# Optimization experiments

Measured on AMD Instinct MI355X. Metric: run time of the kernel, lower is better.

## Reference

```python
import jax, jax.numpy as jnp
import numpy as np

B, S, D_MODEL = 2, 2048, 2048
N_HEADS, N_KV_HEADS = 32, 8
HEAD_DIM = D_MODEL // N_HEADS  # 64


def setup_inputs() -> dict:
    key = jax.random.key(0)
    ks = jax.random.split(key, 7)
    # rope frequencies (as in standard RoPE; values just need to be the right shape)
    inv_freq = 1.0 / (10000.0 ** (jnp.arange(0, HEAD_DIM, 2, dtype=jnp.float32) / HEAD_DIM))
    t = jnp.arange(S, dtype=jnp.float32)
    freqs = t[:, None] * inv_freq[None, :]  # (S, head_dim//2)
    scale = 0.02
    return {
        "x": jax.random.normal(ks[0], (B, S, D_MODEL), jnp.float32),
        "cos": jnp.cos(freqs),
        "sin": jnp.sin(freqs),
        "Wq": jax.random.normal(ks[1], (N_HEADS * HEAD_DIM, D_MODEL), jnp.float32) * scale,
        "Wk": jax.random.normal(ks[2], (N_KV_HEADS * HEAD_DIM, D_MODEL), jnp.float32) * scale,
        "Wv": jax.random.normal(ks[3], (N_KV_HEADS * HEAD_DIM, D_MODEL), jnp.float32) * scale,
        "Wo": jax.random.normal(ks[4], (D_MODEL, D_MODEL), jnp.float32) * scale,
    }


def _apply_rope(x, cos, sin):
    # x: (B, H, S, D); cos/sin: (S, D//2)
    d = x.shape[-1]
    x1, x2 = x[..., : d // 2], x[..., d // 2:]
    c = cos[None, None]
    s = sin[None, None]
    return jnp.concatenate([x1 * c - x2 * s, x1 * s + x2 * c], axis=-1)


def reference(x, cos, sin, Wq, Wk, Wv, Wo):
    b, s, _ = x.shape
    hd = 2 * cos.shape[-1]
    h = Wq.shape[0] // hd
    kv = Wk.shape[0] // hd
    g = h // kv  # query heads per kv head

    q = (x @ Wq.T).reshape(b, s, h, hd).transpose(0, 2, 1, 3)    # (b,h,s,d)
    k = (x @ Wk.T).reshape(b, s, kv, hd).transpose(0, 2, 1, 3)   # (b,kv,s,d)
    v = (x @ Wv.T).reshape(b, s, kv, hd).transpose(0, 2, 1, 3)

    q = _apply_rope(q, cos, sin)
    k = _apply_rope(k, cos, sin)

    # GQA: group query heads instead of materializing repeated K/V
    qg = q.reshape(b, kv, g, s, hd)
    scale = 1.0 / jnp.sqrt(jnp.asarray(hd, x.dtype))
    scores = jnp.einsum('bkgsd,bktd->bkgst', qg, k) * scale      # (b,kv,g,s,s)
    causal = jnp.arange(s)[:, None] >= jnp.arange(s)[None, :]
    scores = jnp.where(causal[None, None, None], scores, jnp.asarray(-jnp.inf, scores.dtype))
    attn = jax.nn.softmax(scores, axis=-1)
    out = jnp.einsum('bkgst,bktd->bkgsd', attn, v)               # (b,kv,g,s,d)
    out = out.reshape(b, h, s, hd).transpose(0, 2, 1, 3).reshape(b, s, h * hd)
    return out @ Wo.T
```

## Files before the change

### kernel.cpp

```cpp
#include <hip/hip_runtime.h>
#include <hip/hip_bf16.h>

typedef __bf16 bf16;
typedef __attribute__((ext_vector_type(8))) __bf16 bf16x8;
typedef __attribute__((ext_vector_type(4))) __bf16 bf16x4;
typedef __attribute__((ext_vector_type(4))) float f32x4;

#define B_SZ 2
#define S_SZ 2048
#define D_SZ 2048
#define H_SZ 32
#define KV_SZ 8
#define HD_SZ 64
#define M_SZ (B_SZ * S_SZ)
#define NQKV 3072

#define GLDS(g, s) __builtin_amdgcn_global_load_lds( \
    (const __attribute__((address_space(1))) void*)(g), \
    (__attribute__((address_space(3))) void*)(s), 16, 0, 0)

__global__ void cvt_all(const float* __restrict__ x, const float* __restrict__ Wq,
                        const float* __restrict__ Wk, const float* __restrict__ Wv,
                        bf16* __restrict__ xb, bf16* __restrict__ Wf,
                        int nx, int n1, int n2) {
    int i = blockIdx.x * blockDim.x + threadIdx.x;
    const float* src; bf16* dst; int off;
    if (i < nx)                { src = x;  dst = xb; off = i; }
    else {
        int j = i - nx;
        if (j < n1)            { src = Wq; dst = Wf; off = j; }
        else if (j < n1 + n2)  { src = Wk; dst = Wf + (size_t)4 * n1; off = j - n1; }
        else if (j < n1+2*n2)  { src = Wv; dst = Wf + (size_t)4 * (n1 + n2); off = j - n1 - n2; }
        else return;
    }
    float4 v = ((const float4*)src)[off];
    bf16x4 o;
    o.x = (bf16)v.x; o.y = (bf16)v.y; o.z = (bf16)v.z; o.w = (bf16)v.w;
    ((bf16x4*)dst)[off] = o;
}

__global__ void cvt_f32_bf16(const float* __restrict__ in, bf16* __restrict__ out, int n4) {
    int i = blockIdx.x * blockDim.x + threadIdx.x;
    if (i >= n4) return;
    float4 v = ((const float4*)in)[i];
    bf16x4 o;
    o.x = (bf16)v.x; o.y = (bf16)v.y; o.z = (bf16)v.z; o.w = (bf16)v.w;
    ((bf16x4*)out)[i] = o;
}

#define BK 64

#define GEMM_CORE(A_, B_, Kdim)                                                  \
    const int g8 = lane >> 3;                                                    \
    const int chs = ((lane & 7) ^ g8) * 8;                                       \
    const bf16* Ag = A_ + (size_t)(rowBase + g8) * Kdim + chs;                   \
    const bf16* Bg = B_ + (size_t)(colBase + g8) * Kdim + chs;                   \
    f32x4 acc[4][4] = {};                                                        \
    for (int k0 = 0; k0 < Kdim; k0 += BK) {                                      \
        _Pragma("unroll")                                                        \
        for (int j = 0; j < 4; j++) {                                            \
            int is = wave * 4 + j;                                               \
            GLDS(Ag + (size_t)(is * 8) * Kdim + k0, As + is * 512);              \
            GLDS(Bg + (size_t)(is * 8) * Kdim + k0, Bs + is * 512);              \
        }                                                                        \
        __syncthreads();                                                         \
        _Pragma("unroll")                                                        \
        for (int ks = 0; ks < 2; ks++) {                                         \
            bf16x8 af[4], bfr[4];                                                \
            _Pragma("unroll")                                                    \
            for (int mi = 0; mi < 4; mi++)                                       \
                af[mi] = *(const bf16x8*)(As + (waveM * 64 + mi * 16 + c) * 64   \
                                          + (((ks << 2) + quad) ^ (c & 7)) * 8); \
            _Pragma("unroll")                                                    \
            for (int ni = 0; ni < 4; ni++)                                       \
                bfr[ni] = *(const bf16x8*)(Bs + (waveN * 64 + ni * 16 + c) * 64  \
                                          + (((ks << 2) + quad) ^ (c & 7)) * 8); \
            _Pragma("unroll")                                                    \
            for (int mi = 0; mi < 4; mi++)                                       \
                _Pragma("unroll")                                                \
                for (int ni = 0; ni < 4; ni++)                                   \
                    acc[mi][ni] = __builtin_amdgcn_mfma_f32_16x16x32_bf16(       \
                        af[mi], bfr[ni], acc[mi][ni], 0, 0, 0);                  \
        }                                                                        \
        __syncthreads();                                                         \
    }

__global__ __launch_bounds__(256)
void gemm_qkv(const bf16* __restrict__ A, const bf16* __restrict__ Bw,
              bf16* __restrict__ Qb, bf16* __restrict__ Kb, bf16* __restrict__ Vtb,
              const float* __restrict__ cosp, const float* __restrict__ sinp,
              float qscale)
{
    __shared__ __align__(16) bf16 As[128 * BK];
    __shared__ __align__(16) bf16 Bs[128 * BK];
    const int tid  = threadIdx.x;
    const int lane = tid & 63;
    const int wave = tid >> 6;
    const int waveM = wave >> 1, waveN = wave & 1;
    const int c = lane & 15, quad = lane >> 4;
    const int rowBase = blockIdx.y * 128;
    const int colBase = blockIdx.x * 128;

    GEMM_CORE(A, Bw, D_SZ)

    const int mBase = rowBase + waveM * 64;
    const int nBase = colBase + waveN * 64;

    if (nBase < 2560) {
        bf16* dst; int hh, Hn; float sc;
        if (nBase < 2048) { dst = Qb; hh = nBase >> 6;        Hn = H_SZ;  sc = qscale; }
        else              { dst = Kb; hh = (nBase >> 6) - 32; Hn = KV_SZ; sc = 1.0f;  }
#pragma unroll
        for (int mi = 0; mi < 4; mi++) {
#pragma unroll
            for (int r = 0; r < 4; r++) {
                int row = mBase + mi * 16 + quad * 4 + r;
                int b = row >> 11;
                int s = row & 2047;
                const float* cr = cosp + (size_t)s * 32;
                const float* sr = sinp + (size_t)s * 32;
                size_t base = ((size_t)(b * Hn + hh) * S_SZ + s) * 64;
#pragma unroll
                for (int ni = 0; ni < 2; ni++) {
                    int d = ni * 16 + c;
                    float x1 = acc[mi][ni][r];
                    float x2 = acc[mi][ni + 2][r];
                    float cv = cr[d], sv = sr[d];
                    dst[base + d]      = (bf16)((x1 * cv - x2 * sv) * sc);
                    dst[base + d + 32] = (bf16)((x1 * sv + x2 * cv) * sc);
                }
            }
        }
    } else {
        const int kvh = (nBase >> 6) - 40;
        const int b   = mBase >> 11;
        const int s0  = mBase & 2047;
#pragma unroll
        for (int ni = 0; ni < 4; ni++) {
            int d = ni * 16 + c;
            size_t base = ((size_t)(b * KV_SZ + kvh) * 64 + d) * (size_t)S_SZ;
#pragma unroll
            for (int mi = 0; mi < 4; mi++) {
                int s = s0 + mi * 16 + quad * 4;
#pragma unroll
                for (int r = 0; r < 4; r++)
                    Vtb[base + s + r] = (bf16)acc[mi][ni][r];
            }
        }
    }
}

__global__ __launch_bounds__(256)
void gemm_out(const bf16* __restrict__ A, const bf16* __restrict__ Bw,
              float* __restrict__ Co, int N, int K)
{
    __shared__ __align__(16) bf16 As[128 * BK];
    __shared__ __align__(16) bf16 Bs[128 * BK];
    const int tid  = threadIdx.x;
    const int lane = tid & 63;
    const int wave = tid >> 6;
    const int waveM = wave >> 1, waveN = wave & 1;
    const int c = lane & 15, quad = lane >> 4;
    const int rowBase = blockIdx.y * 128;
    const int colBase = blockIdx.x * 128;

    GEMM_CORE(A, Bw, K)

    const int mBase = rowBase + waveM * 64;
    const int nBase = colBase + waveN * 64;
#pragma unroll
    for (int mi = 0; mi < 4; mi++)
#pragma unroll
        for (int ni = 0; ni < 4; ni++) {
            int col = nBase + ni * 16 + c;
#pragma unroll
            for (int r = 0; r < 4; r++) {
                int row = mBase + mi * 16 + quad * 4 + r;
                Co[(size_t)row * N + col] = acc[mi][ni][r];
            }
        }
}

#define LDF 72

__global__ __launch_bounds__(256, 2)
void flash_attn(const bf16* __restrict__ Q, const bf16* __restrict__ Kc,
                const bf16* __restrict__ Vt, bf16* __restrict__ Aout)
{
    __shared__ __align__(16) bf16 Ks[64 * LDF];
    __shared__ __align__(16) bf16 Vs[64 * LDF];
    __shared__ __align__(16) bf16 Ps[4 * 16 * LDF];

    const int tid  = threadIdx.x;
    const int lane = tid & 63;
    const int wave = tid >> 6;
    const int c = lane & 15, quad = lane >> 4;
    const int qloc = wave * 16 + c;

    const int i  = blockIdx.x;
    const int tA = 31 - i, tB = i;
    const int q0A = tA << 6, q0B = tB << 6;

    const int bh = blockIdx.y;
    const int b  = bh >> 5;
    const int h  = bh & 31;
    const int kv = h >> 2;

    const bf16* Qp = Q  + (size_t)bh * (S_SZ * 64);
    const bf16* Kp = Kc + (size_t)(b * KV_SZ + kv) * (S_SZ * 64);
    const bf16* Vp = Vt + (size_t)(b * KV_SZ + kv) * (64 * S_SZ);

    bf16x8 aqA[2], aqB[2];
    {
        const bf16* qa = Qp + (size_t)(q0A + qloc) * 64 + quad * 8;
        aqA[0] = *(const bf16x8*)qa;  aqA[1] = *(const bf16x8*)(qa + 32);
        const bf16* qb = Qp + (size_t)(q0B + qloc) * 64 + quad * 8;
        aqB[0] = *(const bf16x8*)qb;  aqB[1] = *(const bf16x8*)(qb + 32);
    }

    f32x4 oA[4] = {}, oB[4] = {};
    f32x4 lA = {}, lB = {};

    bf16x8 ones;
#pragma unroll
    for (int j = 0; j < 8; j++) ones[j] = (bf16)1.0f;

    const int srow = tid >> 3;
    const int soff = (tid & 7) * 8;
    const bf16* Kg0 = Kp + (size_t)srow * 64 + soff;
    const bf16* Kg1 = Kp + (size_t)(srow + 32) * 64 + soff;
    const bf16* Vg0 = Vp + (size_t)srow * S_SZ + soff;
    const bf16* Vg1 = Vp + (size_t)(srow + 32) * S_SZ + soff;

    uint4 pk0 = *(const uint4*)Kg0, pk1 = *(const uint4*)Kg1;
    uint4 pv0 = *(const uint4*)Vg0, pv1 = *(const uint4*)Vg1;

    bf16* Pw = Ps + wave * 16 * LDF;

    for (int kt = 0; kt <= tA; kt++) {
        *(uint4*)(Ks + srow * LDF + soff)        = pk0;
        *(uint4*)(Ks + (srow + 32) * LDF + soff) = pk1;
        *(uint4*)(Vs + srow * LDF + soff)        = pv0;
        *(uint4*)(Vs + (srow + 32) * LDF + soff) = pv1;
        __syncthreads();
        if (kt < tA) {
            pk0 = *(const uint4*)(Kg0 + (size_t)(kt + 1) * 4096);
            pk1 = *(const uint4*)(Kg1 + (size_t)(kt + 1) * 4096);
            pv0 = *(const uint4*)(Vg0 + (kt + 1) * 64);
            pv1 = *(const uint4*)(Vg1 + (kt + 1) * 64);
        }

        bf16x8 ak[2][4], av[2][4];
#pragma unroll
        for (int ks = 0; ks < 2; ks++)
#pragma unroll
            for (int ni = 0; ni < 4; ni++) {
                ak[ks][ni] = *(const bf16x8*)(Ks + (ni * 16 + c) * LDF + ks * 32 + quad * 8);
                av[ks][ni] = *(const bf16x8*)(Vs + (ni * 16 + c) * LDF + ks * 32 + quad * 8);
            }

        const bool diagA = (kt == tA);
        const bool doB   = (kt <= tB);
        const bool diagB = (kt == tB);

        {
            f32x4 sc[4] = {};
#pragma unroll
            for (int ks = 0; ks < 2; ks++)
#pragma unroll
                for (int ni = 0; ni < 4; ni++)
                    sc[ni] = __builtin_amdgcn_mfma_f32_16x16x32_bf16(ak[ks][ni], aqA[ks], sc[ni], 0, 0, 0);
#pragma unroll
            for (int ni = 0; ni < 4; ni++) {
                bf16x4 pk;
#pragma unroll
                for (int r = 0; r < 4; r++) {
                    float p = exp2f(sc[ni][r]);
                    if (diagA && (ni * 16 + quad * 4 + r) > qloc) p = 0.f;
                    pk[r] = (bf16)p;
                }
                *(bf16x4*)(Pw + c * LDF + ni * 16 + quad * 4) = pk;
            }
#pragma unroll
            for (int ks = 0; ks < 2; ks++) {
                bf16x8 bp = *(const bf16x8*)(Pw + c * LDF + ks * 32 + quad * 8);
                lA = __builtin_amdgcn_mfma_f32_16x16x32_bf16(ones, bp, lA, 0, 0, 0);
#pragma unroll
                for (int ni = 0; ni < 4; ni++)
                    oA[ni] = __builtin_amdgcn_mfma_f32_16x16x32_bf16(av[ks][ni], bp, oA[ni], 0, 0, 0);
            }
        }
        if (doB) {
            f32x4 sc[4] = {};
#pragma unroll
            for (int ks = 0; ks < 2; ks++)
#pragma unroll
                for (int ni = 0; ni < 4; ni++)
                    sc[ni] = __builtin_amdgcn_mfma_f32_16x16x32_bf16(ak[ks][ni], aqB[ks], sc[ni], 0, 0, 0);
#pragma unroll
            for (int ni = 0; ni < 4; ni++) {
                bf16x4 pk;
#pragma unroll
                for (int r = 0; r < 4; r++) {
                    float p = exp2f(sc[ni][r]);
                    if (diagB && (ni * 16 + quad * 4 + r) > qloc) p = 0.f;
                    pk[r] = (bf16)p;
                }
                *(bf16x4*)(Pw + c * LDF + ni * 16 + quad * 4) = pk;
            }
#pragma unroll
            for (int ks = 0; ks < 2; ks++) {
                bf16x8 bp = *(const bf16x8*)(Pw + c * LDF + ks * 32 + quad * 8);
                lB = __builtin_amdgcn_mfma_f32_16x16x32_bf16(ones, bp, lB, 0, 0, 0);
#pragma unroll
                for (int ni = 0; ni < 4; ni++)
                    oB[ni] = __builtin_amdgcn_mfma_f32_16x16x32_bf16(av[ks][ni], bp, oB[ni], 0, 0, 0);
            }
        }
        __syncthreads();
    }

    {
        float ila = 1.f / lA[0];
        float ilb = 1.f / lB[0];
        bf16* pa = Aout + ((size_t)(b * S_SZ + q0A + qloc)) * D_SZ + h * 64;
        bf16* pb = Aout + ((size_t)(b * S_SZ + q0B + qloc)) * D_SZ + h * 64;
#pragma unroll
        for (int ni = 0; ni < 4; ni++) {
            bf16x4 wa, wb;
#pragma unroll
            for (int r = 0; r < 4; r++) {
                wa[r] = (bf16)(oA[ni][r] * ila);
                wb[r] = (bf16)(oB[ni][r] * ilb);
            }
            *(bf16x4*)(pa + ni * 16 + quad * 4) = wa;
            *(bf16x4*)(pb + ni * 16 + quad * 4) = wb;
        }
    }
}

extern "C" void kernel_launch(void* const* d_in, const int* in_sizes, int n_in,
                              void* d_out, int out_size, void* d_ws, size_t ws_size,
                              hipStream_t stream) {
    const float* x    = (const float*)d_in[0];
    const float* cosp = (const float*)d_in[1];
    const float* sinp = (const float*)d_in[2];
    const float* Wq   = (const float*)d_in[3];
    const float* Wk   = (const float*)d_in[4];
    const float* Wv   = (const float*)d_in[5];
    const float* Wo   = (const float*)d_in[6];
    float* out = (float*)d_out;

    const int M = M_SZ;
    const int D = D_SZ;
    const int NKV = KV_SZ * HD_SZ;

    bf16* xb   = (bf16*)d_ws;
    bf16* Wf   = xb  + (size_t)M * D;
    bf16* Qb   = Wf  + (size_t)NQKV * D;
    bf16* Kb   = Qb  + (size_t)M * D;
    bf16* Vtb  = Kb  + (size_t)B_SZ * KV_SZ * S_SZ * 64;
    bf16* attn = xb;
    bf16* wob  = Wf;

    const int nx = M * D / 4, n1 = D * D / 4, n2 = NKV * D / 4;

    cvt_all<<<(nx + n1 + 2 * n2 + 255) / 256, 256, 0, stream>>>(x, Wq, Wk, Wv, xb, Wf, nx, n1, n2);

    const float qscale = 0.125f * 1.44269504089f;

    gemm_qkv<<<dim3(NQKV / 128, M / 128), 256, 0, stream>>>(xb, Wf, Qb, Kb, Vtb, cosp, sinp, qscale);

    cvt_f32_bf16<<<(n1 + 255) / 256, 256, 0, stream>>>(Wo, wob, n1);

    flash_attn<<<dim3(16, B_SZ * H_SZ), 256, 0, stream>>>(Qb, Kb, Vtb, attn);

    gemm_out<<<dim3(D / 128, M / 128), 256, 0, stream>>>(attn, wob, out, D, D);
}
```

Baseline: 313.2 us.

## Use two waves per GEMM block with 64x128 per-wave tiles

Both GEMMs change from four waves each computing a 64x64 sub-tile to two waves each computing a 64x128 sub-tile of the same 128x128 block tile. Each wave loads 64 rows of A and B into LDS and reads all 128 B rows, which raises MFMA work per LDS fragment load and doubles accumulator registers per thread. Launch bounds become (128,2). The aim is better register-level reuse, at the cost of fewer waves per block to hide latency and higher register pressure.

```diff
diff --git a/kernel.cpp b/kernel.cpp
--- a/kernel.cpp
+++ b/kernel.cpp
@@ -48,131 +48,123 @@
     ((bf16x4*)out)[i] = o;
 }
 
-#define BK 64
-
-#define GEMM_CORE(A_, B_, Kdim)                                                  \
+#define GEMM_CORE2(A_, B_, Kdim)                                                 \
+    const int tid  = threadIdx.x;                                                \
+    const int w    = tid >> 6;                                                   \
+    const int lane = tid & 63;                                                   \
+    const int c = lane & 15, quad = lane >> 4;                                   \
     const int g8 = lane >> 3;                                                    \
     const int chs = ((lane & 7) ^ g8) * 8;                                       \
-    const bf16* Ag = A_ + (size_t)(rowBase + g8) * Kdim + chs;                   \
-    const bf16* Bg = B_ + (size_t)(colBase + g8) * Kdim + chs;                   \
-    f32x4 acc[4][4] = {};                                                        \
-    for (int k0 = 0; k0 < Kdim; k0 += BK) {                                      \
+    const int rowBase = blockIdx.y * 128;                                        \
+    const int colBase = blockIdx.x * 128;                                        \
+    const bf16* Ag = A_ + (size_t)(rowBase + w * 64 + g8) * Kdim + chs;          \
+    const bf16* Bg = B_ + (size_t)(colBase + w * 64 + g8) * Kdim + chs;          \
+    bf16* sAw = As + (w * 64) * 64;                                              \
+    bf16* sBw = Bs + (w * 64) * 64;                                              \
+    f32x4 acc[4][8] = {};                                                        \
+    for (int k0 = 0; k0 < Kdim; k0 += 64) {                                      \
         _Pragma("unroll")                                                        \
-        for (int j = 0; j < 4; j++) {                                            \
-            int is = wave * 4 + j;                                               \
-            GLDS(Ag + (size_t)(is * 8) * Kdim + k0, As + is * 512);              \
-            GLDS(Bg + (size_t)(is * 8) * Kdim + k0, Bs + is * 512);              \
+        for (int j = 0; j < 8; j++) {                                            \
+            GLDS(Ag + (size_t)(j * 8) * Kdim + k0, sAw + j * 512);               \
+            GLDS(Bg + (size_t)(j * 8) * Kdim + k0, sBw + j * 512);               \
         }                                                                        \
         __syncthreads();                                                         \
         _Pragma("unroll")                                                        \
         for (int ks = 0; ks < 2; ks++) {                                         \
-            bf16x8 af[4], bfr[4];                                                \
+            bf16x8 af[4], bfr[8];                                                \
             _Pragma("unroll")                                                    \
             for (int mi = 0; mi < 4; mi++)                                       \
-                af[mi] = *(const bf16x8*)(As + (waveM * 64 + mi * 16 + c) * 64   \
+                af[mi] = *(const bf16x8*)(As + (w * 64 + mi * 16 + c) * 64       \
                                           + (((ks << 2) + quad) ^ (c & 7)) * 8); \
             _Pragma("unroll")                                                    \
-            for (int ni = 0; ni < 4; ni++)                                       \
-                bfr[ni] = *(const bf16x8*)(Bs + (waveN * 64 + ni * 16 + c) * 64  \
+            for (int ni = 0; ni < 8; ni++)                                       \
+                bfr[ni] = *(const bf16x8*)(Bs + (ni * 16 + c) * 64               \
                                           + (((ks << 2) + quad) ^ (c & 7)) * 8); \
             _Pragma("unroll")                                                    \
             for (int mi = 0; mi < 4; mi++)                                       \
                 _Pragma("unroll")                                                \
-                for (int ni = 0; ni < 4; ni++)                                   \
+                for (int ni = 0; ni < 8; ni++)                                   \
                     acc[mi][ni] = __builtin_amdgcn_mfma_f32_16x16x32_bf16(       \
                         af[mi], bfr[ni], acc[mi][ni], 0, 0, 0);                  \
         }                                                                        \
         __syncthreads();                                                         \
-    }
-
-__global__ __launch_bounds__(256)
+    }                                                                            \
+    const int mBase = rowBase + w * 64;
+
+__global__ __launch_bounds__(128, 2)
 void gemm_qkv(const bf16* __restrict__ A, const bf16* __restrict__ Bw,
               bf16* __restrict__ Qb, bf16* __restrict__ Kb, bf16* __restrict__ Vtb,
               const float* __restrict__ cosp, const float* __restrict__ sinp,
               float qscale)
 {
-    __shared__ __align__(16) bf16 As[128 * BK];
-    __shared__ __align__(16) bf16 Bs[128 * BK];
-    const int tid  = threadIdx.x;
-    const int lane = tid & 63;
-    const int wave = tid >> 6;
-    const int waveM = wave >> 1, waveN = wave & 1;
-    const int c = lane & 15, quad = lane >> 4;
-    const int rowBase = blockIdx.y * 128;
-    const int colBase = blockIdx.x * 128;
-
-    GEMM_CORE(A, Bw, D_SZ)
-
-    const int mBase = rowBase + waveM * 64;
-    const int nBase = colBase + waveN * 64;
-
-    if (nBase < 2560) {
-        bf16* dst; int hh, Hn; float sc;
-        if (nBase < 2048) { dst = Qb; hh = nBase >> 6;        Hn = H_SZ;  sc = qscale; }
-        else              { dst = Kb; hh = (nBase >> 6) - 32; Hn = KV_SZ; sc = 1.0f;  }
-#pragma unroll
-        for (int mi = 0; mi < 4; mi++) {
-#pragma unroll
-            for (int r = 0; r < 4; r++) {
-                int row = mBase + mi * 16 + quad * 4 + r;
-                int b = row >> 11;
-                int s = row & 2047;
-                const float* cr = cosp + (size_t)s * 32;
-                const float* sr = sinp + (size_t)s * 32;
-                size_t base = ((size_t)(b * Hn + hh) * S_SZ + s) * 64;
-#pragma unroll
-                for (int ni = 0; ni < 2; ni++) {
-                    int d = ni * 16 + c;
-                    float x1 = acc[mi][ni][r];
-                    float x2 = acc[mi][ni + 2][r];
-                    float cv = cr[d], sv = sr[d];
-                    dst[base + d]      = (bf16)((x1 * cv - x2 * sv) * sc);
-                    dst[base + d + 32] = (bf16)((x1 * sv + x2 * cv) * sc);
+    __shared__ __align__(16) bf16 As[128 * 64];
+    __shared__ __align__(16) bf16 Bs[128 * 64];
+
+    GEMM_CORE2(A, Bw, D_SZ)
+
+#pragma unroll
+    for (int half = 0; half < 2; half++) {
+        const int hcol = colBase + half * 64;
+        const int no   = half * 4;
+        if (hcol < 2560) {
+            bf16* dst; int hh, Hn; float sc;
+            if (hcol < 2048) { dst = Qb; hh = hcol >> 6;        Hn = H_SZ;  sc = qscale; }
+            else             { dst = Kb; hh = (hcol >> 6) - 32; Hn = KV_SZ; sc = 1.0f;  }
+#pragma unroll
+            for (int mi = 0; mi < 4; mi++) {
+#pragma unroll
+                for (int r = 0; r < 4; r++) {
+                    int row = mBase + mi * 16 + quad * 4 + r;
+                    int b = row >> 11;
+                    int s = row & 2047;
+                    const float* cr = cosp + (size_t)s * 32;
+                    const float* sr = sinp + (size_t)s * 32;
+                    size_t base = ((size_t)(b * Hn + hh) * S_SZ + s) * 64;
+#pragma unroll
+                    for (int nj = 0; nj < 2; nj++) {
+                        int d = nj * 16 + c;
+                        float x1 = acc[mi][no + nj][r];
+                        float x2 = acc[mi][no + nj + 2][r];
+                        float cv = cr[d], sv = sr[d];
+                        dst[base + d]      = (bf16)((x1 * cv - x2 * sv) * sc);
+                        dst[base + d + 32] = (bf16)((x1 * sv + x2 * cv) * sc);
+                    }
                 }
             }
-        }
-    } else {
-        const int kvh = (nBase >> 6) - 40;
-        const int b   = mBase >> 11;
-        const int s0  = mBase & 2047;
-#pragma unroll
-        for (int ni = 0; ni < 4; ni++) {
-            int d = ni * 16 + c;
-            size_t base = ((size_t)(b * KV_SZ + kvh) * 64 + d) * (size_t)S_SZ;
-#pragma unroll
-            for (int mi = 0; mi < 4; mi++) {
-                int s = s0 + mi * 16 + quad * 4;
-#pragma unroll
-                for (int r = 0; r < 4; r++)
-                    Vtb[base + s + r] = (bf16)acc[mi][ni][r];
-            }
-        }
-    }
-}
-
-__global__ __launch_bounds__(256)
+        } else {
+            const int kvh = (hcol >> 6) - 40;
+            const int b   = mBase >> 11;
+            const int s0  = mBase & 2047;
+#pragma unroll
+            for (int nj = 0; nj < 4; nj++) {
+                int d = nj * 16 + c;
+                size_t base = ((size_t)(b * KV_SZ + kvh) * 64 + d) * (size_t)S_SZ;
+#pragma unroll
+                for (int mi = 0; mi < 4; mi++) {
+                    int s = s0 + mi * 16 + quad * 4;
+#pragma unroll
+                    for (int r = 0; r < 4; r++)
+                        Vtb[base + s + r] = (bf16)acc[mi][no + nj][r];
+                }
+            }
+        }
+    }
+}
+
+__global__ __launch_bounds__(128, 2)
 void gemm_out(const bf16* __restrict__ A, const bf16* __restrict__ Bw,
               float* __restrict__ Co, int N, int K)
 {
-    __shared__ __align__(16) bf16 As[128 * BK];
-    __shared__ __align__(16) bf16 Bs[128 * BK];
-    const int tid  = threadIdx.x;
-    const int lane = tid & 63;
-    const int wave = tid >> 6;
-    const int waveM = wave >> 1, waveN = wave & 1;
-    const int c = lane & 15, quad = lane >> 4;
-    const int rowBase = blockIdx.y * 128;
-    const int colBase = blockIdx.x * 128;
-
-    GEMM_CORE(A, Bw, K)
-
-    const int mBase = rowBase + waveM * 64;
-    const int nBase = colBase + waveN * 64;
+    __shared__ __align__(16) bf16 As[128 * 64];
+    __shared__ __align__(16) bf16 Bs[128 * 64];
+
+    GEMM_CORE2(A, Bw, K)
+
 #pragma unroll
     for (int mi = 0; mi < 4; mi++)
 #pragma unroll
-        for (int ni = 0; ni < 4; ni++) {
-            int col = nBase + ni * 16 + c;
+        for (int ni = 0; ni < 8; ni++) {
+            int col = colBase + ni * 16 + c;
 #pragma unroll
             for (int r = 0; r < 4; r++) {
                 int row = mBase + mi * 16 + quad * 4 + r;
@@ -369,11 +361,11 @@
 
     const float qscale = 0.125f * 1.44269504089f;
 
-    gemm_qkv<<<dim3(NQKV / 128, M / 128), 256, 0, stream>>>(xb, Wf, Qb, Kb, Vtb, cosp, sinp, qscale);
+    gemm_qkv<<<dim3(NQKV / 128, M / 128), 128, 0, stream>>>(xb, Wf, Qb, Kb, Vtb, cosp, sinp, qscale);
 
     cvt_f32_bf16<<<(n1 + 255) / 256, 256, 0, stream>>>(Wo, wob, n1);
 
     flash_attn<<<dim3(16, B_SZ * H_SZ), 256, 0, stream>>>(Qb, Kb, Vtb, attn);
 
-    gemm_out<<<dim3(D / 128, M / 128), 256, 0, stream>>>(attn, wob, out, D, D);
-}
+    gemm_out<<<dim3(D / 128, M / 128), 128, 0, stream>>>(attn, wob, out, D, D);
+}
```

New measurement: 295.6 us. -5.6%, faster.
